# Optimization experiments

Measured on AMD Instinct MI355X. Metric: run time of the kernel, lower is better.

The kernel has to match this reference:

```python
import jax, jax.numpy as jnp
import numpy as np

N_HEAD = 16
SPARSE_TOPK = 64
NEG_INF = float('-inf')


def setup_inputs() -> dict:
    key = jax.random.key(0)
    ks = jax.random.split(key, 12)
    B, T, C = 4, 1024, 1024
    s = 0.02
    q = jax.random.normal(ks[0], (B, T, C), jnp.float32)
    kv = jax.random.normal(ks[1], (B, T, C), jnp.float32)  # forward asserts k == v
    tgt_mask = jnp.tril(jnp.ones((T, T), jnp.bool_)).reshape(1, 1, T, T)
    inp = {'q': q, 'k': kv, 'v': kv, 'tgt_mask': tgt_mask}
    for i, n in enumerate(['Wq', 'Wk', 'Wv', 'Wo']):
        inp[n] = jax.random.normal(ks[2 + i], (C, C), jnp.float32) * s
    for i, n in enumerate(['bq', 'bk', 'bv', 'bo']):
        inp[n] = jax.random.normal(ks[6 + i], (C,), jnp.float32) * s
    return inp


def reference(q, k, v, tgt_mask, Wq, Wk, Wv, Wo, bq, bk, bv, bo):
    B, T, C = q.shape
    H = N_HEAD
    hd = C // H
    scale = 1.0 / np.sqrt(hd).astype(np.float32)
    # QKV projections -> [B, H, T, hd]
    qh = (q @ Wq + bq).reshape(B, T, H, hd).transpose(0, 2, 1, 3)
    kh = (k @ Wk + bk).reshape(B, T, H, hd).transpose(0, 2, 1, 3)
    vh = (v @ Wv + bv).reshape(B, T, H, hd).transpose(0, 2, 1, 3)
    # full attention scores [B, H, T, T]
    att = jnp.einsum('bhtd,bhsd->bhts', qh, kh) * scale
    # causal mask: masked_fill where tgt_mask == 0
    att = jnp.where(tgt_mask[:, :, :T, :T], att, NEG_INF)
    # top-k sparse pruning: keep entries >= k-th largest per row (ties kept)
    top, _ = jax.lax.top_k(att, SPARSE_TOPK)
    vk = top[..., -1:]  # [B, H, T, 1]
    att = jnp.where(att < vk, NEG_INF, att)
    att = jax.nn.softmax(att, axis=-1)
    # dropout is identity in eval (p=0.0)
    y = jnp.einsum('bhts,bhsd->bhtd', att, vh)
    y = y.transpose(0, 2, 1, 3).reshape(B, T, C)
    return y @ Wo + bo
```

## Files before the change

kernel.cpp:

```cpp
#include <hip/hip_runtime.h>
#include <hip/hip_bf16.h>
#include <math.h>

typedef __attribute__((ext_vector_type(8))) short short8;
typedef __attribute__((ext_vector_type(4))) float f32x4;
typedef __attribute__((ext_vector_type(4))) int int4v;

#define SCL 0.1803368801111204f

static __device__ __forceinline__ unsigned short f2bf(float f) {
  unsigned u = __float_as_uint(f);
  u = u + 0x7FFFu + ((u >> 16) & 1u);
  return (unsigned short)(u >> 16);
}

static __device__ __forceinline__ unsigned keyof(float x) {
  unsigned u = __float_as_uint(x);
  return (u & 0x80000000u) ? ~u : (u | 0x80000000u);
}
static __device__ __forceinline__ float keyinv(unsigned k) {
  unsigned u = (k & 0x80000000u) ? (k & 0x7FFFFFFFu) : ~k;
  return __uint_as_float(u);
}

static __device__ __forceinline__ int saddr(int r, int cc) {
  return (((r << 9) + cc) << 2) ^ ((r & 7) << 4);
}
static __device__ __forceinline__ int paddr(int r, int c) {
  return ((r << 11) + (c << 1)) ^ ((r & 7) << 4);
}

static __device__ __forceinline__ void gld_lds16(const unsigned short* g, unsigned short* l) {
  __builtin_amdgcn_global_load_lds(
      (const __attribute__((address_space(1))) void*)g,
      (__attribute__((address_space(3))) void*)l, 16, 0, 0);
}

__global__ __launch_bounds__(256) void cvt3_k(const float* __restrict__ q,
                                              const float* __restrict__ k,
                                              const float* __restrict__ v,
                                              unsigned short* __restrict__ oq,
                                              unsigned short* __restrict__ ok,
                                              unsigned short* __restrict__ ov) {
  const int y = blockIdx.y;
  const float* in = (y == 0) ? q : (y == 1) ? k : v;
  unsigned short* out = (y == 0) ? oq : (y == 1) ? ok : ov;
  const int i = blockIdx.x * 256 + threadIdx.x;
  const f32x4* p = (const f32x4*)in + 2 * (size_t)i;
  f32x4 a = p[0], b = p[1];
  short8 r;
  r[0] = (short)f2bf(a[0]); r[1] = (short)f2bf(a[1]);
  r[2] = (short)f2bf(a[2]); r[3] = (short)f2bf(a[3]);
  r[4] = (short)f2bf(b[0]); r[5] = (short)f2bf(b[1]);
  r[6] = (short)f2bf(b[2]); r[7] = (short)f2bf(b[3]);
  ((short8*)out)[i] = r;
}

__global__ __launch_bounds__(256) void wtrans4_k(const float* __restrict__ Wq,
                                                 const float* __restrict__ Wk,
                                                 const float* __restrict__ Wv,
                                                 const float* __restrict__ Wo,
                                                 unsigned short* __restrict__ Wqt,
                                                 unsigned short* __restrict__ Wkt,
                                                 unsigned short* __restrict__ Wvt,
                                                 unsigned short* __restrict__ Wot) {
  const int z = blockIdx.z;
  const float* W = (z == 0) ? Wq : (z == 1) ? Wk : (z == 2) ? Wv : Wo;
  unsigned short* Wt = (z == 0) ? Wqt : (z == 1) ? Wkt : (z == 2) ? Wvt : Wot;
  __shared__ float tile[32][33];
  const int tx = threadIdx.x, ty = threadIdx.y;
  const int x0 = blockIdx.x * 32, y0 = blockIdx.y * 32;
#pragma unroll
  for (int j = 0; j < 4; ++j)
    tile[ty + j * 8][tx] = W[(y0 + ty + j * 8) * 1024 + x0 + tx];
  __syncthreads();
#pragma unroll
  for (int j = 0; j < 4; ++j)
    Wt[(x0 + ty + j * 8) * 1024 + (y0 + tx)] = f2bf(tile[tx][ty + j * 8]);
}

template <int MODE>
static __device__ __forceinline__ void gemm_body(unsigned short* As0, unsigned short* Bs0,
                                                 unsigned short* As1, unsigned short* Bs1,
                                                 const unsigned short* __restrict__ A,
                                                 const unsigned short* __restrict__ Bt,
                                                 const float* __restrict__ bias,
                                                 void* __restrict__ out) {
  const int tid = threadIdx.x;
  const int lane = tid & 63, w = tid >> 6;
  const int wr = w >> 1, wc = w & 1;
  const int m0 = blockIdx.y * 128, n0 = blockIdx.x * 128;
  const int l15 = lane & 15, l4 = lane >> 4;
  f32x4 acc[4][4] = {};
  const int r0 = tid >> 2, s0 = (tid & 3) * 8;
  const int r1 = r0 + 64;
  const unsigned short* gA0 = A + (m0 + r0) * 1024 + s0;
  const unsigned short* gA1 = A + (m0 + r1) * 1024 + s0;
  const unsigned short* gB0 = Bt + (n0 + r0) * 1024 + s0;
  const unsigned short* gB1 = Bt + (n0 + r1) * 1024 + s0;
  const int oA0 = r0 * 32 + s0, oA1 = r1 * 32 + s0;

  gld_lds16(gA0, As0 + oA0);
  gld_lds16(gA1, As0 + oA1);
  gld_lds16(gB0, Bs0 + oA0);
  gld_lds16(gB1, Bs0 + oA1);
  __syncthreads();

  for (int kt = 0; kt < 32; ++kt) {
    if (kt < 31) {
      const int k0n = (kt + 1) * 32;
      unsigned short* Asn = (kt & 1) ? As0 : As1;
      unsigned short* Bsn = (kt & 1) ? Bs0 : Bs1;
      gld_lds16(gA0 + k0n, Asn + oA0);
      gld_lds16(gA1 + k0n, Asn + oA1);
      gld_lds16(gB0 + k0n, Bsn + oA0);
      gld_lds16(gB1 + k0n, Bsn + oA1);
    }
    const unsigned short* Asc = (kt & 1) ? As1 : As0;
    const unsigned short* Bsc = (kt & 1) ? Bs1 : Bs0;
    short8 af[4], bfr[4];
#pragma unroll
    for (int i = 0; i < 4; ++i) {
      af[i]  = *(const short8*)(Asc + (wr * 64 + i * 16 + l15) * 32 + l4 * 8);
      bfr[i] = *(const short8*)(Bsc + (wc * 64 + i * 16 + l15) * 32 + l4 * 8);
    }
#pragma unroll
    for (int i = 0; i < 4; ++i)
#pragma unroll
      for (int j = 0; j < 4; ++j)
        acc[i][j] = __builtin_amdgcn_mfma_f32_16x16x32_bf16(af[i], bfr[j], acc[i][j], 0, 0, 0);
    __syncthreads();
  }
#pragma unroll
  for (int i = 0; i < 4; ++i) {
#pragma unroll
    for (int j = 0; j < 4; ++j) {
      const int n = n0 + wc * 64 + j * 16 + l15;
      const float bv = bias[n];
#pragma unroll
      for (int r = 0; r < 4; ++r) {
        const int m = m0 + wr * 64 + i * 16 + l4 * 4 + r;
        const float v = acc[i][j][r] + bv;
        if (MODE == 2) {
          ((float*)out)[m * 1024 + n] = v;
        } else {
          const int bb = m >> 10, t = m & 1023, hh = n >> 6, dd = n & 63;
          const unsigned short bfv = f2bf(v);
          if (MODE == 0)
            ((unsigned short*)out)[(((bb << 4) + hh) * 1024 + t) * 64 + dd] = bfv;
          else
            ((unsigned short*)out)[(((bb << 4) + hh) * 64 + dd) * 1024 + t] = bfv;
        }
      }
    }
  }
}

__global__ __launch_bounds__(256) void gemm_qkv_k(
    const unsigned short* qbf, const unsigned short* kbf, const unsigned short* vbf,
    const unsigned short* Wqt, const unsigned short* Wkt, const unsigned short* Wvt,
    const float* bq, const float* bk, const float* bv,
    unsigned short* Qh, unsigned short* Kh, unsigned short* Vth) {
  __shared__ unsigned short As0[128 * 32], Bs0[128 * 32], As1[128 * 32], Bs1[128 * 32];
  const int z = blockIdx.z;
  const unsigned short* A  = (z == 0) ? qbf : ((z == 1) ? kbf : vbf);
  const unsigned short* Bt = (z == 0) ? Wqt : ((z == 1) ? Wkt : Wvt);
  const float* bias        = (z == 0) ? bq  : ((z == 1) ? bk  : bv);
  if (z == 2) gemm_body<1>(As0, Bs0, As1, Bs1, A, Bt, bias, Vth);
  else        gemm_body<0>(As0, Bs0, As1, Bs1, A, Bt, bias, z ? Kh : Qh);
}

__global__ __launch_bounds__(256) void gemm_out_k(const unsigned short* Y,
                                                  const unsigned short* Wot,
                                                  const float* bo, float* out) {
  __shared__ unsigned short As0[128 * 32], Bs0[128 * 32], As1[128 * 32], Bs1[128 * 32];
  gemm_body<2>(As0, Bs0, As1, Bs1, Y, Wot, bo, out);
}

template <int NVAL>
static __device__ __forceinline__ void process_row(char* __restrict__ smem, float (&v)[NVAL],
                                                   const int r, const int Lr, const int Lpad,
                                                   const int lane, float* __restrict__ RED2) {
  float lm = v[0];
#pragma unroll
  for (int i = 1; i < NVAL; ++i) lm = fmaxf(lm, v[i]);
  float mx = lm;
#pragma unroll
  for (int o = 32; o; o >>= 1) mx = fmaxf(mx, __shfl_xor(mx, o));

  float thr = -INFINITY;
  if (Lr > 64) {
    float mn = lm;
#pragma unroll
    for (int o = 32; o; o >>= 1) mn = fminf(mn, __shfl_xor(mn, o));
    unsigned lo = (unsigned)__builtin_amdgcn_readfirstlane((int)keyof(mn));
    unsigned hi = (unsigned)__builtin_amdgcn_readfirstlane((int)keyof(mx)) + 1u;
    int cl = Lr, ch = 0, alt = 0;
    while (hi - lo > 1u) {
      const unsigned span = hi - lo;
      unsigned off;
      if (alt) off = span >> 1;
      else {
        const float fr = (float)(cl - 64) / (float)(cl - ch);
        off = (unsigned)(fr * (float)span);
        if (off < 1u) off = 1u;
        if (off > span - 1u) off = span - 1u;
      }
      alt ^= 1;
      const unsigned mid = lo + off;
      const float tm = keyinv(mid);
      int cnt = 0;
#pragma unroll
      for (int i = 0; i < NVAL; ++i) cnt += (int)__popcll(__ballot(v[i] >= tm));
      if (cnt >= 64) { lo = mid; cl = cnt; if (cnt == 64) break; }
      else { hi = mid; ch = cnt; }
    }
    thr = keyinv(lo);
  }

  float s = 0.f;
  unsigned pk[NVAL / 2];
#pragma unroll
  for (int p = 0; p < NVAL / 2; ++p) {
    const float p0 = (v[2 * p]     >= thr) ? exp2f(v[2 * p]     - mx) : 0.f;
    const float p1 = (v[2 * p + 1] >= thr) ? exp2f(v[2 * p + 1] - mx) : 0.f;
    s += p0 + p1;
    pk[p] = (unsigned)f2bf(p0) | ((unsigned)f2bf(p1) << 16);
  }
#pragma unroll
  for (int o = 32; o; o >>= 1) s += __shfl_xor(s, o);
  if (lane == 0) RED2[r] = 1.f / s;
#pragma unroll
  for (int p = 0; p < NVAL / 2; ++p) {
    const int c = ((p & 3) << 7) + (lane << 1) + ((p >= 4) ? 512 : 0);
    if (c < Lpad) *(unsigned*)(smem + paddr(r, c)) = pk[p];
  }
}

template <int NVAL>
static __device__ __forceinline__ void attn_body(char* __restrict__ smem,
                                                 const unsigned short* __restrict__ Qp,
                                                 const unsigned short* __restrict__ Kh,
                                                 const unsigned short* __restrict__ Vh,
                                                 unsigned short* __restrict__ Y,
                                                 const int t0, const int h, const int b,
                                                 const int lane, const int w) {
  const int L = t0 + 16;
  const int Lpad = (L + 31) & ~31;
  const int nCT = L >> 4;
  const int l15 = lane & 15, l4 = lane >> 4;
  float* RED  = (float*)(smem + 32768);
  float* RED2 = (float*)(smem + 32768 + 4352);

  const short8 aq0 = *(const short8*)(Qp + l15 * 64 + l4 * 8);
  const short8 aq1 = *(const short8*)(Qp + l15 * 64 + 32 + l4 * 8);

  auto qk_chunk = [&](int tlo, int thi) {
    for (int ct = tlo + w; ct < thi; ct += 8) {
      const int c0 = ct * 16;
      const short8 kb0 = *(const short8*)(Kh + (c0 + l15) * 64 + l4 * 8);
      const short8 kb1 = *(const short8*)(Kh + (c0 + l15) * 64 + 32 + l4 * 8);
      f32x4 acc = {0.f, 0.f, 0.f, 0.f};
      acc = __builtin_amdgcn_mfma_f32_16x16x32_bf16(aq0, kb0, acc, 0, 0, 0);
      acc = __builtin_amdgcn_mfma_f32_16x16x32_bf16(aq1, kb1, acc, 0, 0, 0);
      const int c = c0 + l15, cc = c & 511;
      if (ct == nCT - 1) {
#pragma unroll
        for (int r = 0; r < 4; ++r) {
          const int row = l4 * 4 + r;
          *(float*)(smem + saddr(row, cc)) = (c <= t0 + row) ? acc[r] * SCL : -INFINITY;
        }
      } else {
#pragma unroll
        for (int r = 0; r < 4; ++r)
          *(float*)(smem + saddr(l4 * 4 + r, cc)) = acc[r] * SCL;
      }
    }
  };

  qk_chunk(0, (nCT < 32) ? nCT : 32);
  __syncthreads();

  const int rA = w * 2, rB = rA + 1;
  const int LrA = t0 + rA + 1, LrB = t0 + rB + 1;
  float vA[NVAL], vB[NVAL];
#pragma unroll
  for (int p = 0; p < 4; ++p) {
    const int c = (p << 7) + (lane << 1);
    const float2 tA = *(const float2*)(smem + saddr(rA, c));
    const float2 tB = *(const float2*)(smem + saddr(rB, c));
    const bool vld = c < L;
    vA[2 * p]     = vld ? tA.x : -INFINITY;
    vA[2 * p + 1] = vld ? tA.y : -INFINITY;
    vB[2 * p]     = vld ? tB.x : -INFINITY;
    vB[2 * p + 1] = vld ? tB.y : -INFINITY;
  }

  if constexpr (NVAL == 16) {
    __syncthreads();
    qk_chunk(32, nCT);
    __syncthreads();
#pragma unroll
    for (int p = 0; p < 4; ++p) {
      const int cc = (p << 7) + (lane << 1);
      const float2 tA = *(const float2*)(smem + saddr(rA, cc));
      const bool vld = (cc + 512) < L;
      vA[8 + 2 * p] = vld ? tA.x : -INFINITY;
      vA[9 + 2 * p] = vld ? tA.y : -INFINITY;
    }
    process_row<NVAL>(smem, vA, rA, LrA, Lpad, lane, RED2);
#pragma unroll
    for (int p = 0; p < 4; ++p) {
      const int cc = (p << 7) + (lane << 1);
      const float2 tB = *(const float2*)(smem + saddr(rB, cc));
      const bool vld = (cc + 512) < L;
      vB[8 + 2 * p] = vld ? tB.x : -INFINITY;
      vB[9 + 2 * p] = vld ? tB.y : -INFINITY;
    }
    process_row<NVAL>(smem, vB, rB, LrB, Lpad, lane, RED2);
  } else {
    process_row<NVAL>(smem, vA, rA, LrA, Lpad, lane, RED2);
    process_row<NVAL>(smem, vB, rB, LrB, Lpad, lane, RED2);
  }
  __syncthreads();

  const int nST = Lpad >> 5;
  const int stMid = (nST + 1) >> 1;
  const int d0 = (w & 3) * 16;
  const int stLo = (w < 4) ? 0 : stMid;
  const int stHi = (w < 4) ? stMid : nST;
  f32x4 acc = {0.f, 0.f, 0.f, 0.f};
  for (int st = stLo; st < stHi; ++st) {
    const int sb = st * 32 + l4 * 8;
    const short8 paf = *(const short8*)(smem + paddr(l15, sb));
    const short8 vb = *(const short8*)(Vh + (d0 + l15) * 1024 + sb);
    acc = __builtin_amdgcn_mfma_f32_16x16x32_bf16(paf, vb, acc, 0, 0, 0);
  }
  if (w >= 4) {
    const int base = (w - 4) * 272 + l15;
#pragma unroll
    for (int r = 0; r < 4; ++r) RED[base + (l4 * 4 + r) * 17] = acc[r];
  }
  __syncthreads();
  if (w < 4) {
    const int base = w * 272 + l15;
    const int d = (h << 6) + d0 + l15;
#pragma unroll
    for (int r = 0; r < 4; ++r) {
      const float inv = RED2[l4 * 4 + r];
      const float vr = (acc[r] + RED[base + (l4 * 4 + r) * 17]) * inv;
      const int tg = t0 + l4 * 4 + r;
      Y[((b << 10) + tg) * 1024 + d] = f2bf(vr);
    }
  }
}

__global__ __launch_bounds__(512, 6) void attn_k(const unsigned short* __restrict__ Q,
                                                 const unsigned short* __restrict__ K,
                                                 const unsigned short* __restrict__ Vt,
                                                 unsigned short* __restrict__ Y) {
  extern __shared__ __align__(16) char smem[];
  const int tid = threadIdx.x, lane = tid & 63, w = tid >> 6;
  const int t0 = (63 - (int)blockIdx.x) * 16;
  const int h = blockIdx.y, b = blockIdx.z;
  const unsigned short* Qp = Q + (((b * 16 + h) * 1024) + t0) * 64;
  const unsigned short* Kh = K + (b * 16 + h) * 65536;
  const unsigned short* Vh = Vt + (b * 16 + h) * 65536;
  if (t0 >= 512) attn_body<16>(smem, Qp, Kh, Vh, Y, t0, h, b, lane, w);
  else           attn_body<8>(smem, Qp, Kh, Vh, Y, t0, h, b, lane, w);
}

extern "C" void kernel_launch(void* const* d_in, const int* in_sizes, int n_in,
                              void* d_out, int out_size, void* d_ws, size_t ws_size,
                              hipStream_t stream) {
  const float* q  = (const float*)d_in[0];
  const float* k  = (const float*)d_in[1];
  const float* v  = (const float*)d_in[2];
  const float* Wq = (const float*)d_in[4];
  const float* Wk = (const float*)d_in[5];
  const float* Wv = (const float*)d_in[6];
  const float* Wo = (const float*)d_in[7];
  const float* bq = (const float*)d_in[8];
  const float* bk = (const float*)d_in[9];
  const float* bv = (const float*)d_in[10];
  const float* bo = (const float*)d_in[11];

  char* ws = (char*)d_ws;
  const size_t MB = 1u << 20;
  unsigned short* qbf = (unsigned short*)(ws + 0 * MB);
  unsigned short* kbf = (unsigned short*)(ws + 8 * MB);
  unsigned short* vbf = (unsigned short*)(ws + 16 * MB);
  unsigned short* Wqt = (unsigned short*)(ws + 24 * MB);
  unsigned short* Wkt = (unsigned short*)(ws + 26 * MB);
  unsigned short* Wvt = (unsigned short*)(ws + 28 * MB);
  unsigned short* Wot = (unsigned short*)(ws + 30 * MB);
  unsigned short* Qh  = (unsigned short*)(ws + 32 * MB);
  unsigned short* Kh  = (unsigned short*)(ws + 40 * MB);
  unsigned short* Vth = (unsigned short*)(ws + 48 * MB);
  unsigned short* Y   = qbf;

  cvt3_k<<<dim3(2048, 3), 256, 0, stream>>>(q, k, v, qbf, kbf, vbf);
  wtrans4_k<<<dim3(32, 32, 4), dim3(32, 8), 0, stream>>>(Wq, Wk, Wv, Wo, Wqt, Wkt, Wvt, Wot);
  gemm_qkv_k<<<dim3(8, 32, 3), 256, 0, stream>>>(qbf, kbf, vbf, Wqt, Wkt, Wvt,
                                                 bq, bk, bv, Qh, Kh, Vth);
  attn_k<<<dim3(64, 16, 4), 512, 37248, stream>>>(Qh, Kh, Vth, Y);
  gemm_out_k<<<dim3(8, 32), 256, 0, stream>>>(Y, Wot, bo, (float*)d_out);
}
```

Measured before the change: 211.3 us.

## Use 1024-thread attention blocks with one row per wave and DPP reductions

The attention kernel moves from 512 to 1024 threads, so each of 16 waves handles one query row instead of two. The PV product is split four ways along the key dimension, with partial sums reduced through a larger LDS buffer. Cross-lane max/min/sum reductions now use DPP moves for the intra-row steps, and the top-k threshold search gets a bounded iteration count. The aim is more parallelism and a shorter serial softmax/top-k path per wave, at the cost of more LDS, heavier barriers and register pressure under the new launch bounds.

Result: slower. 219.2 us (+3.7%).

```diff
diff --git a/kernel.cpp b/kernel.cpp
--- a/kernel.cpp
+++ b/kernel.cpp
@@ -21,6 +21,31 @@
 static __device__ __forceinline__ float keyinv(unsigned k) {
   unsigned u = (k & 0x80000000u) ? (k & 0x7FFFFFFFu) : ~k;
   return __uint_as_float(u);
+}
+
+#define DPP_RED_STEP(x, OP, CTRL) \
+  x = OP(x, __int_as_float(__builtin_amdgcn_mov_dpp(__float_as_int(x), CTRL, 0xf, 0xf, true)))
+static __device__ __forceinline__ void red_maxmin(float& mx, float& mn) {
+  DPP_RED_STEP(mx, fmaxf, 0xB1); DPP_RED_STEP(mn, fminf, 0xB1);
+  DPP_RED_STEP(mx, fmaxf, 0x4E); DPP_RED_STEP(mn, fminf, 0x4E);
+  DPP_RED_STEP(mx, fmaxf, 0x141); DPP_RED_STEP(mn, fminf, 0x141);
+  DPP_RED_STEP(mx, fmaxf, 0x140); DPP_RED_STEP(mn, fminf, 0x140);
+  mx = fmaxf(mx, __shfl_xor(mx, 16)); mn = fminf(mn, __shfl_xor(mn, 16));
+  mx = fmaxf(mx, __shfl_xor(mx, 32)); mn = fminf(mn, __shfl_xor(mn, 32));
+}
+static __device__ __forceinline__ float red_sum(float s) {
+  DPP_RED_STEP(s, __builtin_fmaf(1.f, 0.f, 0.f) + , 0);
+  return s;
+}
+#undef DPP_RED_STEP
+static __device__ __forceinline__ float red_sum2(float s) {
+#define DPP_ADD(x, CTRL) \
+  x = x + __int_as_float(__builtin_amdgcn_mov_dpp(__float_as_int(x), CTRL, 0xf, 0xf, true))
+  DPP_ADD(s, 0xB1); DPP_ADD(s, 0x4E); DPP_ADD(s, 0x141); DPP_ADD(s, 0x140);
+#undef DPP_ADD
+  s += __shfl_xor(s, 16);
+  s += __shfl_xor(s, 32);
+  return s;
 }
 
 static __device__ __forceinline__ int saddr(int r, int cc) {
@@ -177,26 +202,104 @@
   gemm_body<2>(As0, Bs0, As1, Bs1, Y, Wot, bo, out);
 }
 
-template <int NVAL>
-static __device__ __forceinline__ void process_row(char* __restrict__ smem, float (&v)[NVAL],
-                                                   const int r, const int Lr, const int Lpad,
-                                                   const int lane, float* __restrict__ RED2) {
+__global__ __launch_bounds__(1024, 8) void attn_k(const unsigned short* __restrict__ Q,
+                                                  const unsigned short* __restrict__ K,
+                                                  const unsigned short* __restrict__ Vt,
+                                                  unsigned short* __restrict__ Y) {
+  extern __shared__ __align__(16) char smem[];
+  const int tid = threadIdx.x, lane = tid & 63, w = tid >> 6;
+  const int t0 = 1008 - 16 * (int)blockIdx.x;
+  const int h = blockIdx.y, b = blockIdx.z;
+  const unsigned short* Qp = Q + (((b * 16 + h) * 1024) + t0) * 64;
+  const unsigned short* Kh = K + (b * 16 + h) * 65536;
+  const unsigned short* Vh = Vt + (b * 16 + h) * 65536;
+  const int L = t0 + 16;
+  const int Lpad = (L + 31) & ~31;
+  const int nCT = L >> 4;
+  const bool full = (L > 512);
+  const int l15 = lane & 15, l4 = lane >> 4;
+  float* RED3 = (float*)(smem + 32768);
+  float* RED2 = (float*)(smem + 32768 + 13056);
+
+  const short8 aq0 = *(const short8*)(Qp + l15 * 64 + l4 * 8);
+  const short8 aq1 = *(const short8*)(Qp + l15 * 64 + 32 + l4 * 8);
+
+  auto qk_tiles = [&](int tlo, int thi) {
+    for (int ct = tlo + w; ct < thi; ct += 16) {
+      const int c0 = ct * 16;
+      const short8 kb0 = *(const short8*)(Kh + (c0 + l15) * 64 + l4 * 8);
+      const short8 kb1 = *(const short8*)(Kh + (c0 + l15) * 64 + 32 + l4 * 8);
+      f32x4 acc = {0.f, 0.f, 0.f, 0.f};
+      acc = __builtin_amdgcn_mfma_f32_16x16x32_bf16(aq0, kb0, acc, 0, 0, 0);
+      acc = __builtin_amdgcn_mfma_f32_16x16x32_bf16(aq1, kb1, acc, 0, 0, 0);
+      const int c = c0 + l15, cc = c & 511;
+      if (ct == nCT - 1) {
+#pragma unroll
+        for (int r = 0; r < 4; ++r) {
+          const int row = l4 * 4 + r;
+          *(float*)(smem + saddr(row, cc)) = (c <= t0 + row) ? acc[r] * SCL : -INFINITY;
+        }
+      } else {
+#pragma unroll
+        for (int r = 0; r < 4; ++r)
+          *(float*)(smem + saddr(l4 * 4 + r, cc)) = acc[r] * SCL;
+      }
+    }
+  };
+
+  qk_tiles(0, full ? 32 : nCT);
+  __syncthreads();
+
+  const int Lr = t0 + w + 1;
+  float v[16];
+#pragma unroll
+  for (int p = 0; p < 4; ++p) {
+    const int c = (p << 7) + (lane << 1);
+    const float2 t = *(const float2*)(smem + saddr(w, c));
+    const bool vld = full || (c < L);
+    v[2 * p]     = vld ? t.x : -INFINITY;
+    v[2 * p + 1] = vld ? t.y : -INFINITY;
+  }
+  if (full) {
+    __syncthreads();
+    qk_tiles(32, nCT);
+    __syncthreads();
+#pragma unroll
+    for (int p = 0; p < 4; ++p) {
+      const int cc = (p << 7) + (lane << 1);
+      const float2 t = *(const float2*)(smem + saddr(w, cc));
+      const bool vld = (cc + 512) < L;
+      v[8 + 2 * p] = vld ? t.x : -INFINITY;
+      v[9 + 2 * p] = vld ? t.y : -INFINITY;
+    }
+  } else {
+#pragma unroll
+    for (int i = 8; i < 16; ++i) v[i] = -INFINITY;
+  }
+
   float lm = v[0];
 #pragma unroll
-  for (int i = 1; i < NVAL; ++i) lm = fmaxf(lm, v[i]);
-  float mx = lm;
-#pragma unroll
-  for (int o = 32; o; o >>= 1) mx = fmaxf(mx, __shfl_xor(mx, o));
+  for (int i = 1; i < 16; ++i) lm = fmaxf(lm, v[i]);
+  float mx = lm, mn = lm;
+  red_maxmin(mx, mn);
+
+  auto countge = [&](float tm) {
+    int cnt = 0;
+#pragma unroll
+    for (int i = 0; i < 8; ++i) cnt += (int)__popcll(__ballot(v[i] >= tm));
+    if (full) {
+#pragma unroll
+      for (int i = 8; i < 16; ++i) cnt += (int)__popcll(__ballot(v[i] >= tm));
+    }
+    return cnt;
+  };
 
   float thr = -INFINITY;
   if (Lr > 64) {
-    float mn = lm;
-#pragma unroll
-    for (int o = 32; o; o >>= 1) mn = fminf(mn, __shfl_xor(mn, o));
     unsigned lo = (unsigned)__builtin_amdgcn_readfirstlane((int)keyof(mn));
     unsigned hi = (unsigned)__builtin_amdgcn_readfirstlane((int)keyof(mx)) + 1u;
     int cl = Lr, ch = 0, alt = 0;
-    while (hi - lo > 1u) {
+    for (int it = 0; it < 64 && (hi - lo) > 1u; ++it) {
       const unsigned span = hi - lo;
       unsigned off;
       if (alt) off = span >> 1;
@@ -208,166 +311,78 @@
       }
       alt ^= 1;
       const unsigned mid = lo + off;
-      const float tm = keyinv(mid);
-      int cnt = 0;
-#pragma unroll
-      for (int i = 0; i < NVAL; ++i) cnt += (int)__popcll(__ballot(v[i] >= tm));
-      if (cnt >= 64) { lo = mid; cl = cnt; if (cnt == 64) break; }
+      const int cnt = countge(keyinv(mid));
+      if (cnt >= 64) { lo = mid; cl = cnt; if (cnt == 64) hi = mid + 1u; }
       else { hi = mid; ch = cnt; }
     }
     thr = keyinv(lo);
   }
 
   float s = 0.f;
-  unsigned pk[NVAL / 2];
-#pragma unroll
-  for (int p = 0; p < NVAL / 2; ++p) {
+  unsigned pk[8];
+#pragma unroll
+  for (int p = 0; p < 4; ++p) {
     const float p0 = (v[2 * p]     >= thr) ? exp2f(v[2 * p]     - mx) : 0.f;
     const float p1 = (v[2 * p + 1] >= thr) ? exp2f(v[2 * p + 1] - mx) : 0.f;
     s += p0 + p1;
     pk[p] = (unsigned)f2bf(p0) | ((unsigned)f2bf(p1) << 16);
   }
-#pragma unroll
-  for (int o = 32; o; o >>= 1) s += __shfl_xor(s, o);
-  if (lane == 0) RED2[r] = 1.f / s;
-#pragma unroll
-  for (int p = 0; p < NVAL / 2; ++p) {
-    const int c = ((p & 3) << 7) + (lane << 1) + ((p >= 4) ? 512 : 0);
-    if (c < Lpad) *(unsigned*)(smem + paddr(r, c)) = pk[p];
-  }
-}
-
-template <int NVAL>
-static __device__ __forceinline__ void attn_body(char* __restrict__ smem,
-                                                 const unsigned short* __restrict__ Qp,
-                                                 const unsigned short* __restrict__ Kh,
-                                                 const unsigned short* __restrict__ Vh,
-                                                 unsigned short* __restrict__ Y,
-                                                 const int t0, const int h, const int b,
-                                                 const int lane, const int w) {
-  const int L = t0 + 16;
-  const int Lpad = (L + 31) & ~31;
-  const int nCT = L >> 4;
-  const int l15 = lane & 15, l4 = lane >> 4;
-  float* RED  = (float*)(smem + 32768);
-  float* RED2 = (float*)(smem + 32768 + 4352);
-
-  const short8 aq0 = *(const short8*)(Qp + l15 * 64 + l4 * 8);
-  const short8 aq1 = *(const short8*)(Qp + l15 * 64 + 32 + l4 * 8);
-
-  auto qk_chunk = [&](int tlo, int thi) {
-    for (int ct = tlo + w; ct < thi; ct += 8) {
-      const int c0 = ct * 16;
-      const short8 kb0 = *(const short8*)(Kh + (c0 + l15) * 64 + l4 * 8);
-      const short8 kb1 = *(const short8*)(Kh + (c0 + l15) * 64 + 32 + l4 * 8);
-      f32x4 acc = {0.f, 0.f, 0.f, 0.f};
-      acc = __builtin_amdgcn_mfma_f32_16x16x32_bf16(aq0, kb0, acc, 0, 0, 0);
-      acc = __builtin_amdgcn_mfma_f32_16x16x32_bf16(aq1, kb1, acc, 0, 0, 0);
-      const int c = c0 + l15, cc = c & 511;
-      if (ct == nCT - 1) {
-#pragma unroll
-        for (int r = 0; r < 4; ++r) {
-          const int row = l4 * 4 + r;
-          *(float*)(smem + saddr(row, cc)) = (c <= t0 + row) ? acc[r] * SCL : -INFINITY;
-        }
-      } else {
-#pragma unroll
-        for (int r = 0; r < 4; ++r)
-          *(float*)(smem + saddr(l4 * 4 + r, cc)) = acc[r] * SCL;
-      }
-    }
-  };
-
-  qk_chunk(0, (nCT < 32) ? nCT : 32);
-  __syncthreads();
-
-  const int rA = w * 2, rB = rA + 1;
-  const int LrA = t0 + rA + 1, LrB = t0 + rB + 1;
-  float vA[NVAL], vB[NVAL];
+  if (full) {
+#pragma unroll
+    for (int p = 4; p < 8; ++p) {
+      const float p0 = (v[2 * p]     >= thr) ? exp2f(v[2 * p]     - mx) : 0.f;
+      const float p1 = (v[2 * p + 1] >= thr) ? exp2f(v[2 * p + 1] - mx) : 0.f;
+      s += p0 + p1;
+      pk[p] = (unsigned)f2bf(p0) | ((unsigned)f2bf(p1) << 16);
+    }
+  }
 #pragma unroll
   for (int p = 0; p < 4; ++p) {
     const int c = (p << 7) + (lane << 1);
-    const float2 tA = *(const float2*)(smem + saddr(rA, c));
-    const float2 tB = *(const float2*)(smem + saddr(rB, c));
-    const bool vld = c < L;
-    vA[2 * p]     = vld ? tA.x : -INFINITY;
-    vA[2 * p + 1] = vld ? tA.y : -INFINITY;
-    vB[2 * p]     = vld ? tB.x : -INFINITY;
-    vB[2 * p + 1] = vld ? tB.y : -INFINITY;
-  }
-
-  if constexpr (NVAL == 16) {
-    __syncthreads();
-    qk_chunk(32, nCT);
-    __syncthreads();
-#pragma unroll
-    for (int p = 0; p < 4; ++p) {
-      const int cc = (p << 7) + (lane << 1);
-      const float2 tA = *(const float2*)(smem + saddr(rA, cc));
-      const bool vld = (cc + 512) < L;
-      vA[8 + 2 * p] = vld ? tA.x : -INFINITY;
-      vA[9 + 2 * p] = vld ? tA.y : -INFINITY;
-    }
-    process_row<NVAL>(smem, vA, rA, LrA, Lpad, lane, RED2);
-#pragma unroll
-    for (int p = 0; p < 4; ++p) {
-      const int cc = (p << 7) + (lane << 1);
-      const float2 tB = *(const float2*)(smem + saddr(rB, cc));
-      const bool vld = (cc + 512) < L;
-      vB[8 + 2 * p] = vld ? tB.x : -INFINITY;
-      vB[9 + 2 * p] = vld ? tB.y : -INFINITY;
-    }
-    process_row<NVAL>(smem, vB, rB, LrB, Lpad, lane, RED2);
-  } else {
-    process_row<NVAL>(smem, vA, rA, LrA, Lpad, lane, RED2);
-    process_row<NVAL>(smem, vB, rB, LrB, Lpad, lane, RED2);
-  }
+    if (c < Lpad) *(unsigned*)(smem + paddr(w, c)) = pk[p];
+  }
+  if (full) {
+#pragma unroll
+    for (int p = 4; p < 8; ++p) {
+      const int c = ((p & 3) << 7) + (lane << 1) + 512;
+      if (c < Lpad) *(unsigned*)(smem + paddr(w, c)) = pk[p];
+    }
+  }
+  s = red_sum2(s);
+  if (lane == 0) RED2[w] = 1.f / s;
   __syncthreads();
 
   const int nST = Lpad >> 5;
-  const int stMid = (nST + 1) >> 1;
+  const int qd = (nST + 3) >> 2;
+  const int kseg = w >> 2;
   const int d0 = (w & 3) * 16;
-  const int stLo = (w < 4) ? 0 : stMid;
-  const int stHi = (w < 4) ? stMid : nST;
+  int klo = kseg * qd, khi = klo + qd;
+  if (klo > nST) klo = nST;
+  if (khi > nST) khi = nST;
   f32x4 acc = {0.f, 0.f, 0.f, 0.f};
-  for (int st = stLo; st < stHi; ++st) {
+  for (int st = klo; st < khi; ++st) {
     const int sb = st * 32 + l4 * 8;
     const short8 paf = *(const short8*)(smem + paddr(l15, sb));
     const short8 vb = *(const short8*)(Vh + (d0 + l15) * 1024 + sb);
     acc = __builtin_amdgcn_mfma_f32_16x16x32_bf16(paf, vb, acc, 0, 0, 0);
   }
-  if (w >= 4) {
-    const int base = (w - 4) * 272 + l15;
-#pragma unroll
-    for (int r = 0; r < 4; ++r) RED[base + (l4 * 4 + r) * 17] = acc[r];
+  if (kseg > 0) {
+#pragma unroll
+    for (int r = 0; r < 4; ++r)
+      RED3[((kseg - 1) * 16 + l4 * 4 + r) * 68 + d0 + l15] = acc[r];
   }
   __syncthreads();
-  if (w < 4) {
-    const int base = w * 272 + l15;
+  if (kseg == 0) {
     const int d = (h << 6) + d0 + l15;
 #pragma unroll
     for (int r = 0; r < 4; ++r) {
-      const float inv = RED2[l4 * 4 + r];
-      const float vr = (acc[r] + RED[base + (l4 * 4 + r) * 17]) * inv;
-      const int tg = t0 + l4 * 4 + r;
-      Y[((b << 10) + tg) * 1024 + d] = f2bf(vr);
-    }
-  }
-}
-
-__global__ __launch_bounds__(512, 6) void attn_k(const unsigned short* __restrict__ Q,
-                                                 const unsigned short* __restrict__ K,
-                                                 const unsigned short* __restrict__ Vt,
-                                                 unsigned short* __restrict__ Y) {
-  extern __shared__ __align__(16) char smem[];
-  const int tid = threadIdx.x, lane = tid & 63, w = tid >> 6;
-  const int t0 = (63 - (int)blockIdx.x) * 16;
-  const int h = blockIdx.y, b = blockIdx.z;
-  const unsigned short* Qp = Q + (((b * 16 + h) * 1024) + t0) * 64;
-  const unsigned short* Kh = K + (b * 16 + h) * 65536;
-  const unsigned short* Vh = Vt + (b * 16 + h) * 65536;
-  if (t0 >= 512) attn_body<16>(smem, Qp, Kh, Vh, Y, t0, h, b, lane, w);
-  else           attn_body<8>(smem, Qp, Kh, Vh, Y, t0, h, b, lane, w);
+      const int row = l4 * 4 + r;
+      const int col = d0 + l15;
+      float sv = acc[r] + RED3[row * 68 + col] + RED3[(16 + row) * 68 + col] +
+                 RED3[(32 + row) * 68 + col];
+      Y[((b << 10) + t0 + row) * 1024 + d] = f2bf(sv * RED2[row]);
+    }
+  }
 }
 
 extern "C" void kernel_launch(void* const* d_in, const int* in_sizes, int n_in,
@@ -403,6 +418,6 @@
   wtrans4_k<<<dim3(32, 32, 4), dim3(32, 8), 0, stream>>>(Wq, Wk, Wv, Wo, Wqt, Wkt, Wvt, Wot);
   gemm_qkv_k<<<dim3(8, 32, 3), 256, 0, stream>>>(qbf, kbf, vbf, Wqt, Wkt, Wvt,
                                                  bq, bk, bv, Qh, Kh, Vth);
-  attn_k<<<dim3(64, 16, 4), 512, 37248, stream>>>(Qh, Kh, Vth, Y);
+  attn_k<<<dim3(64, 16, 4), 1024, 45888, stream>>>(Qh, Kh, Vth, Y);
   gemm_out_k<<<dim3(8, 32), 256, 0, stream>>>(Y, Wot, bo, (float*)d_out);
 }
```
